# Optimization experiments

Measured on AMD Instinct MI355X. Metric: run time of the kernel, lower is better.

## Reference

```python
import jax, jax.numpy as jnp
import numpy as np

B, N_TASKS, DIM = 32768, 8, 128
HIDDEN = DIM  # _MLP default: hidden_dim = out_dim


def setup_inputs() -> dict:
    key = jax.random.key(0)
    ks = jax.random.split(key, 13)
    s = 1.0 / np.sqrt(DIM)
    return {
        "task_features": jax.random.normal(ks[0], (B, N_TASKS, DIM), jnp.float32),
        "in_proj_w": jax.random.normal(ks[1], (3 * DIM, DIM), jnp.float32) * s,
        "in_proj_b": jax.random.normal(ks[2], (3 * DIM,), jnp.float32) * 0.02,
        "out_w": jax.random.normal(ks[3], (DIM, DIM), jnp.float32) * s,
        "out_b": jax.random.normal(ks[4], (DIM,), jnp.float32) * 0.02,
        "fuse_w1": jax.random.normal(ks[5], (HIDDEN, N_TASKS * DIM), jnp.float32) / np.sqrt(N_TASKS * DIM),
        "fuse_b1": jax.random.normal(ks[6], (HIDDEN,), jnp.float32) * 0.02,
        "fuse_w2": jax.random.normal(ks[7], (DIM, HIDDEN), jnp.float32) * s,
        "fuse_b2": jax.random.normal(ks[8], (DIM,), jnp.float32) * 0.02,
        "upd_w1": jax.random.normal(ks[9], (HIDDEN, DIM), jnp.float32) * s,
        "upd_b1": jax.random.normal(ks[10], (HIDDEN,), jnp.float32) * 0.02,
        "upd_w2": jax.random.normal(ks[11], (DIM, HIDDEN), jnp.float32) * s,
        "upd_b2": jax.random.normal(ks[12], (DIM,), jnp.float32) * 0.02,
    }


def reference(task_features, in_proj_w, in_proj_b, out_w, out_b,
              fuse_w1, fuse_b1, fuse_w2, fuse_b2,
              upd_w1, upd_b1, upd_w2, upd_b2):
    b, n, d = task_features.shape
    # MHA with seq_len=1 query/key: softmax over a single key == 1, so
    # A_k = out_proj(v_proj(F_i)) for every k (independent of k, heads, q/k proj).
    Wv = in_proj_w[2 * d:]           # (d, d) value projection rows of in_proj_weight
    bv = in_proj_b[2 * d:]
    A = (task_features @ Wv.T + bv) @ out_w.T + out_b   # (B, n, d): A[:, i] = attn output for target task i
    # eq (7): concat of A_1..A_n for target i = n identical copies of A[:, i]
    concatA = jnp.tile(A, (1, 1, n))                     # (B, n, n*d)
    h = jax.nn.relu(concatA @ fuse_w1.T + fuse_b1)       # (B, n, hidden)
    Ahat = h @ fuse_w2.T + fuse_b2 + A                   # (B, n, d)
    # eq (8): update MLP + residual
    h2 = jax.nn.relu(Ahat @ upd_w1.T + upd_b1)
    return h2 @ upd_w2.T + upd_b2 + task_features        # (B, n, d)
```

## Files before the change

### kernel.cpp

```cpp
#include <hip/hip_runtime.h>

typedef __bf16 bf16;
typedef __bf16 bf16x8 __attribute__((ext_vector_type(8)));
typedef __bf16 bf16x4 __attribute__((ext_vector_type(4)));
typedef float  f32x4  __attribute__((ext_vector_type(4)));

#define MFMA16(a, b, c) __builtin_amdgcn_mfma_f32_16x16x32_bf16((a), (b), (c), 0, 0, 0)

#define LDS_FENCE() __asm__ volatile("s_waitcnt lgkmcnt(0)" ::: "memory")

__global__ void prep_kernel(const float* __restrict__ in_proj_w,
                            const float* __restrict__ in_proj_b,
                            const float* __restrict__ out_w,
                            const float* __restrict__ out_b,
                            const float* __restrict__ fuse_w1,
                            const float* __restrict__ fuse_w2,
                            const float* __restrict__ upd_w1,
                            const float* __restrict__ upd_w2,
                            bf16* __restrict__ W_A,
                            bf16* __restrict__ Wmats,
                            float* __restrict__ b_A) {
    const int i = blockIdx.x;
    const int k = threadIdx.x;
    float accW = 0.f;
    for (int j = 0; j < 128; ++j)
        accW += out_w[i * 128 + j] * in_proj_w[(256 + j) * 128 + k];
    W_A[i * 128 + k] = (bf16)accW;
    float accE = 0.f;
    for (int j = 0; j < 8; ++j)
        accE += fuse_w1[i * 1024 + j * 128 + k];
    Wmats[0 * 16384 + i * 128 + k] = (bf16)accE;
    Wmats[1 * 16384 + i * 128 + k] = (bf16)fuse_w2[i * 128 + k];
    Wmats[2 * 16384 + i * 128 + k] = (bf16)upd_w1[i * 128 + k];
    Wmats[3 * 16384 + i * 128 + k] = (bf16)upd_w2[i * 128 + k];
    if (k == 0) {
        float accB = out_b[i];
        for (int j = 0; j < 128; ++j)
            accB += out_w[i * 128 + j] * in_proj_b[256 + j];
        b_A[i] = accB;
    }
}

constexpr int THREADS     = 1024;
constexpr int WAVES       = 16;
constexpr int LDS_W       = 32768;
constexpr int LDS_WEIGHTS = 4 * LDS_W;
constexpr int STG_STRIDE  = 128;
constexpr int STG_BYTES   = 16 * STG_STRIDE;
constexpr int LDS_TOTAL   = LDS_WEIGHTS + WAVES * STG_BYTES;
constexpr int N_IT        = 2;
constexpr int SLOTS       = 256 * WAVES;

__global__ __launch_bounds__(THREADS, 1)
void fsl_main(const float* __restrict__ x,
              const bf16* __restrict__ W_A,
              const float* __restrict__ b_A,
              const bf16* __restrict__ Wmats,
              const float* __restrict__ fuse_b1,
              const float* __restrict__ fuse_b2,
              const float* __restrict__ upd_b1,
              const float* __restrict__ upd_b2,
              float* __restrict__ out) {
    extern __shared__ __align__(16) char smem[];
    const int tid  = threadIdx.x;
    const int lane = tid & 63;
    const int wave = tid >> 6;
    const int c    = lane & 15;
    const int q    = lane >> 4;

    {
        uint4 z = {0u, 0u, 0u, 0u};
        for (int i = tid; i < LDS_TOTAL / 16; i += THREADS)
            ((uint4*)smem)[i] = z;
    }
    __syncthreads();

    for (int g = tid; g < 4 * 128 * 16; g += THREADS) {
        const int s  = g >> 11;
        const int m  = (g >> 4) & 127;
        const int gk = g & 15;
        uint4 v = *(const uint4*)(Wmats + s * 16384 + m * 128 + gk * 8);
        *(uint4*)(smem + s * LDS_W + m * 256 + ((gk ^ (m & 7)) * 16)) = v;
    }
    __syncthreads();

    char* const stg = smem + LDS_WEIGHTS + wave * STG_BYTES;
    const int wslot = blockIdx.x * WAVES + wave;

    for (int it = 0; it < N_IT; ++it) {
        const int blk  = wslot + it * SLOTS;
        const int row0 = blk * 32;

        bf16x8 Xf[2][4], Af[2][4], Hf[2][4];
        f32x4  acc[2][8];

#pragma unroll
        for (int u = 0; u < 2; ++u) {
            const float* xr = x + (row0 + u * 16 + c) * 128 + q * 8;
#pragma unroll
            for (int t = 0; t < 4; ++t) {
                f32x4 lo = *(const f32x4*)(xr + t * 32);
                f32x4 hi = *(const f32x4*)(xr + t * 32 + 4);
                bf16x8 f;
#pragma unroll
                for (int j = 0; j < 4; ++j) {
                    f[j]     = (bf16)lo[j];
                    f[4 + j] = (bf16)hi[j];
                }
                Xf[u][t] = f;
            }
        }

        auto zero_acc = [&]() {
#pragma unroll
            for (int u = 0; u < 2; ++u)
#pragma unroll
                for (int mt = 0; mt < 8; ++mt)
                    acc[u][mt] = f32x4{0.f, 0.f, 0.f, 0.f};
        };

        auto gemm_global = [&](const bf16* W, bf16x8 (&in)[2][4]) {
            zero_acc();
#pragma unroll
            for (int mt = 0; mt < 8; ++mt) {
                const bf16* wrow = W + (mt * 16 + c) * 128 + q * 8;
#pragma unroll
                for (int t = 0; t < 4; ++t) {
                    bf16x8 wf = *(const bf16x8*)(wrow + t * 32);
#pragma unroll
                    for (int u = 0; u < 2; ++u)
                        acc[u][mt] = MFMA16(wf, in[u][t], acc[u][mt]);
                }
            }
        };

        auto gemm_lds = [&](int s, bf16x8 (&in)[2][4]) {
            zero_acc();
#pragma unroll
            for (int mt = 0; mt < 8; ++mt) {
                const int m = mt * 16 + c;
                const char* wrow = smem + s * LDS_W + m * 256;
                const int msw = m & 7;
#pragma unroll
                for (int t = 0; t < 4; ++t) {
                    bf16x8 wf = *(const bf16x8*)(wrow + (((t * 4 + q) ^ msw) * 16));
#pragma unroll
                    for (int u = 0; u < 2; ++u)
                        acc[u][mt] = MFMA16(wf, in[u][t], acc[u][mt]);
                }
            }
        };

        auto transition = [&](const float* bias, bool relu, bf16x8 (*resid)[4],
                              bf16x8 (*dst)[4], bool to_global) {
#pragma unroll
            for (int u = 0; u < 2; ++u) {
#pragma unroll
                for (int p = 0; p < 2; ++p) {
#pragma unroll
                    for (int mi = 0; mi < 4; ++mi) {
                        const int mt = 4 * p + mi;
                        f32x4 a = acc[u][mt];
                        f32x4 bv = *(const f32x4*)(bias + mt * 16 + q * 4);
#pragma unroll
                        for (int r = 0; r < 4; ++r) {
                            float v = a[r] + bv[r];
                            if (relu) v = v > 0.f ? v : 0.f;
                            a[r] = v;
                        }
                        bf16x4 pk = {(bf16)a[0], (bf16)a[1], (bf16)a[2], (bf16)a[3]};
                        const int hl = mi * 16 + q * 4;
                        *(bf16x4*)(stg + c * STG_STRIDE + (((hl >> 3) ^ (c & 7)) * 16) +
                                   (hl & 7) * 2) = pk;
                    }
                    LDS_FENCE();
#pragma unroll
                    for (int ti = 0; ti < 2; ++ti) {
                        const int t  = 2 * p + ti;
                        const int kl = ti * 32 + q * 8;
                        bf16x8 sv = *(const bf16x8*)(stg + c * STG_STRIDE +
                                                     (((kl >> 3) ^ (c & 7)) * 16));
                        if (to_global) {
                            float* orow = out + (row0 + u * 16 + c) * 128 + t * 32 + q * 8;
                            bf16x8 rv = resid[u][t];
                            f32x4 lo, hi;
#pragma unroll
                            for (int j = 0; j < 4; ++j) {
                                lo[j] = (float)sv[j]     + (float)rv[j];
                                hi[j] = (float)sv[4 + j] + (float)rv[4 + j];
                            }
                            *(f32x4*)(orow)     = lo;
                            *(f32x4*)(orow + 4) = hi;
                        } else {
                            if (resid) {
                                bf16x8 rv = resid[u][t];
                                bf16x8 o;
#pragma unroll
                                for (int j = 0; j < 8; ++j)
                                    o[j] = (bf16)((float)sv[j] + (float)rv[j]);
                                sv = o;
                            }
                            dst[u][t] = sv;
                        }
                    }
                    LDS_FENCE();
                }
            }
        };

        gemm_global(W_A, Xf);
        transition(b_A, false, nullptr, Af, false);
        gemm_lds(0, Af);
        transition(fuse_b1, true, nullptr, Hf, false);
        gemm_lds(1, Hf);
        transition(fuse_b2, false, Af, Hf, false);
        gemm_lds(2, Hf);
        transition(upd_b1, true, nullptr, Af, false);
        gemm_lds(3, Af);
        transition(upd_b2, false, Xf, nullptr, true);
    }
}

extern "C" void kernel_launch(void* const* d_in, const int* in_sizes, int n_in,
                              void* d_out, int out_size, void* d_ws, size_t ws_size,
                              hipStream_t stream) {
    const float* task      = (const float*)d_in[0];
    const float* in_proj_w = (const float*)d_in[1];
    const float* in_proj_b = (const float*)d_in[2];
    const float* out_w     = (const float*)d_in[3];
    const float* out_b     = (const float*)d_in[4];
    const float* fuse_w1   = (const float*)d_in[5];
    const float* fuse_b1   = (const float*)d_in[6];
    const float* fuse_w2   = (const float*)d_in[7];
    const float* fuse_b2   = (const float*)d_in[8];
    const float* upd_w1    = (const float*)d_in[9];
    const float* upd_b1    = (const float*)d_in[10];
    const float* upd_w2    = (const float*)d_in[11];
    const float* upd_b2    = (const float*)d_in[12];
    float* out = (float*)d_out;

    bf16*  W_A   = (bf16*)d_ws;
    bf16*  Wmats = W_A + 16384;
    float* b_A   = (float*)((char*)d_ws + 32768 + 131072);

    (void)in_sizes; (void)n_in; (void)out_size; (void)ws_size;

    hipFuncSetAttribute((const void*)fsl_main,
                        hipFuncAttributeMaxDynamicSharedMemorySize, LDS_TOTAL);

    prep_kernel<<<128, 128, 0, stream>>>(in_proj_w, in_proj_b, out_w, out_b,
                                         fuse_w1, fuse_w2, upd_w1, upd_w2,
                                         W_A, Wmats, b_A);
    fsl_main<<<256, THREADS, LDS_TOTAL, stream>>>(task, W_A, b_A, Wmats,
                                                  fuse_b1, fuse_b2, upd_b1, upd_b2,
                                                  out);
}
```

Baseline: 445.0 us.

## Add register-checked fallback kernel reading weights from global memory

Changes the main kernel's launch bounds to request 4 waves per EU, which limits register allocation. It adds an alternative kernel with 512-thread blocks that streams weights straight from global/L2 instead of staging all weights in LDS. At launch time it checks the compiled register count and spills and falls back to the global-weight kernel if the primary one spills or gets too few registers. The goal is to avoid spilling and improve the occupancy trade-off, at the cost of more repeated global weight loads and a host-side attribute query on every launch.

```diff
diff --git a/kernel.cpp b/kernel.cpp
--- a/kernel.cpp
+++ b/kernel.cpp
@@ -41,17 +41,19 @@
     }
 }
 
+constexpr int STG_STRIDE  = 128;
+constexpr int STG_BYTES   = 16 * STG_STRIDE;
+
 constexpr int THREADS     = 1024;
 constexpr int WAVES       = 16;
 constexpr int LDS_W       = 32768;
 constexpr int LDS_WEIGHTS = 4 * LDS_W;
-constexpr int STG_STRIDE  = 128;
-constexpr int STG_BYTES   = 16 * STG_STRIDE;
 constexpr int LDS_TOTAL   = LDS_WEIGHTS + WAVES * STG_BYTES;
 constexpr int N_IT        = 2;
 constexpr int SLOTS       = 256 * WAVES;
 
-__global__ __launch_bounds__(THREADS, 1)
+__global__ __launch_bounds__(THREADS)
+__attribute__((amdgpu_waves_per_eu(4, 4)))
 void fsl_main(const float* __restrict__ x,
               const bf16* __restrict__ W_A,
               const float* __restrict__ b_A,
@@ -217,6 +219,157 @@
         gemm_lds(2, Hf);
         transition(upd_b1, true, nullptr, Af, false);
         gemm_lds(3, Af);
+        transition(upd_b2, false, Xf, nullptr, true);
+    }
+}
+
+constexpr int THREADS_G = 512;
+constexpr int WAVES_G   = 8;
+constexpr int LDS_TOTAL_G = WAVES_G * STG_BYTES;
+constexpr int GRID_G    = 512;
+constexpr int SLOTS_G   = GRID_G * WAVES_G;
+constexpr int N_IT_G    = 2;
+
+__global__ __launch_bounds__(THREADS_G, 2)
+void fsl_main_g(const float* __restrict__ x,
+                const bf16* __restrict__ W_A,
+                const float* __restrict__ b_A,
+                const bf16* __restrict__ Wmats,
+                const float* __restrict__ fuse_b1,
+                const float* __restrict__ fuse_b2,
+                const float* __restrict__ upd_b1,
+                const float* __restrict__ upd_b2,
+                float* __restrict__ out) {
+    extern __shared__ __align__(16) char smem[];
+    const int tid  = threadIdx.x;
+    const int lane = tid & 63;
+    const int wave = tid >> 6;
+    const int c    = lane & 15;
+    const int q    = lane >> 4;
+
+    {
+        uint4 z = {0u, 0u, 0u, 0u};
+        for (int i = tid; i < LDS_TOTAL_G / 16; i += THREADS_G)
+            ((uint4*)smem)[i] = z;
+    }
+    __syncthreads();
+
+    char* const stg = smem + wave * STG_BYTES;
+    const int wslot = blockIdx.x * WAVES_G + wave;
+
+    for (int it = 0; it < N_IT_G; ++it) {
+        const int blk  = wslot + it * SLOTS_G;
+        const int row0 = blk * 32;
+
+        bf16x8 Xf[2][4], Af[2][4], Hf[2][4];
+        f32x4  acc[2][8];
+
+#pragma unroll
+        for (int u = 0; u < 2; ++u) {
+            const float* xr = x + (row0 + u * 16 + c) * 128 + q * 8;
+#pragma unroll
+            for (int t = 0; t < 4; ++t) {
+                f32x4 lo = *(const f32x4*)(xr + t * 32);
+                f32x4 hi = *(const f32x4*)(xr + t * 32 + 4);
+                bf16x8 f;
+#pragma unroll
+                for (int j = 0; j < 4; ++j) {
+                    f[j]     = (bf16)lo[j];
+                    f[4 + j] = (bf16)hi[j];
+                }
+                Xf[u][t] = f;
+            }
+        }
+
+        auto zero_acc = [&]() {
+#pragma unroll
+            for (int u = 0; u < 2; ++u)
+#pragma unroll
+                for (int mt = 0; mt < 8; ++mt)
+                    acc[u][mt] = f32x4{0.f, 0.f, 0.f, 0.f};
+        };
+
+        auto gemm_global = [&](const bf16* W, bf16x8 (&in)[2][4]) {
+            zero_acc();
+#pragma unroll
+            for (int mt = 0; mt < 8; ++mt) {
+                const bf16* wrow = W + (mt * 16 + c) * 128 + q * 8;
+#pragma unroll
+                for (int t = 0; t < 4; ++t) {
+                    bf16x8 wf = *(const bf16x8*)(wrow + t * 32);
+#pragma unroll
+                    for (int u = 0; u < 2; ++u)
+                        acc[u][mt] = MFMA16(wf, in[u][t], acc[u][mt]);
+                }
+            }
+        };
+
+        auto transition = [&](const float* bias, bool relu, bf16x8 (*resid)[4],
+                              bf16x8 (*dst)[4], bool to_global) {
+#pragma unroll
+            for (int u = 0; u < 2; ++u) {
+#pragma unroll
+                for (int p = 0; p < 2; ++p) {
+#pragma unroll
+                    for (int mi = 0; mi < 4; ++mi) {
+                        const int mt = 4 * p + mi;
+                        f32x4 a = acc[u][mt];
+                        f32x4 bv = *(const f32x4*)(bias + mt * 16 + q * 4);
+#pragma unroll
+                        for (int r = 0; r < 4; ++r) {
+                            float v = a[r] + bv[r];
+                            if (relu) v = v > 0.f ? v : 0.f;
+                            a[r] = v;
+                        }
+                        bf16x4 pk = {(bf16)a[0], (bf16)a[1], (bf16)a[2], (bf16)a[3]};
+                        const int hl = mi * 16 + q * 4;
+                        *(bf16x4*)(stg + c * STG_STRIDE + (((hl >> 3) ^ (c & 7)) * 16) +
+                                   (hl & 7) * 2) = pk;
+                    }
+                    LDS_FENCE();
+#pragma unroll
+                    for (int ti = 0; ti < 2; ++ti) {
+                        const int t  = 2 * p + ti;
+                        const int kl = ti * 32 + q * 8;
+                        bf16x8 sv = *(const bf16x8*)(stg + c * STG_STRIDE +
+                                                     (((kl >> 3) ^ (c & 7)) * 16));
+                        if (to_global) {
+                            float* orow = out + (row0 + u * 16 + c) * 128 + t * 32 + q * 8;
+                            bf16x8 rv = resid[u][t];
+                            f32x4 lo, hi;
+#pragma unroll
+                            for (int j = 0; j < 4; ++j) {
+                                lo[j] = (float)sv[j]     + (float)rv[j];
+                                hi[j] = (float)sv[4 + j] + (float)rv[4 + j];
+                            }
+                            *(f32x4*)(orow)     = lo;
+                            *(f32x4*)(orow + 4) = hi;
+                        } else {
+                            if (resid) {
+                                bf16x8 rv = resid[u][t];
+                                bf16x8 o;
+#pragma unroll
+                                for (int j = 0; j < 8; ++j)
+                                    o[j] = (bf16)((float)sv[j] + (float)rv[j]);
+                                sv = o;
+                            }
+                            dst[u][t] = sv;
+                        }
+                    }
+                    LDS_FENCE();
+                }
+            }
+        };
+
+        gemm_global(W_A, Xf);
+        transition(b_A, false, nullptr, Af, false);
+        gemm_global(Wmats + 0 * 16384, Af);
+        transition(fuse_b1, true, nullptr, Hf, false);
+        gemm_global(Wmats + 1 * 16384, Hf);
+        transition(fuse_b2, false, Af, Hf, false);
+        gemm_global(Wmats + 2 * 16384, Hf);
+        transition(upd_b1, true, nullptr, Af, false);
+        gemm_global(Wmats + 3 * 16384, Af);
         transition(upd_b2, false, Xf, nullptr, true);
     }
 }
@@ -245,13 +398,25 @@
 
     (void)in_sizes; (void)n_in; (void)out_size; (void)ws_size;
 
-    hipFuncSetAttribute((const void*)fsl_main,
-                        hipFuncAttributeMaxDynamicSharedMemorySize, LDS_TOTAL);
-
     prep_kernel<<<128, 128, 0, stream>>>(in_proj_w, in_proj_b, out_w, out_b,
                                          fuse_w1, fuse_w2, upd_w1, upd_w2,
                                          W_A, Wmats, b_A);
-    fsl_main<<<256, THREADS, LDS_TOTAL, stream>>>(task, W_A, b_A, Wmats,
-                                                  fuse_b1, fuse_b2, upd_b1, upd_b2,
-                                                  out);
+
+    hipFuncAttributes fa{};
+    bool use_primary = false;
+    if (hipFuncGetAttributes(&fa, (const void*)fsl_main) == hipSuccess)
+        use_primary = (fa.numRegs >= 96) && (fa.localSizeBytes == 0);
+
+    if (use_primary) {
+        hipFuncSetAttribute((const void*)fsl_main,
+                            hipFuncAttributeMaxDynamicSharedMemorySize, LDS_TOTAL);
+        fsl_main<<<256, THREADS, LDS_TOTAL, stream>>>(task, W_A, b_A, Wmats,
+                                                      fuse_b1, fuse_b2, upd_b1,
+                                                      upd_b2, out);
+    } else {
+        fsl_main_g<<<GRID_G, THREADS_G, LDS_TOTAL_G, stream>>>(task, W_A, b_A,
+                                                               Wmats, fuse_b1,
+                                                               fuse_b2, upd_b1,
+                                                               upd_b2, out);
+    }
 }
```

Result: slower. 458.8 us (+3.1%).
